# Kernel tuning notes

Measured on AMD Instinct MI355X. Metric: run time of the kernel, lower is better.

The kernel has to match this reference:

```python
import jax, jax.numpy as jnp
import numpy as np

N_NODES = 100000
N_EDGES = 2000000
FEAT = 4
H = 64
L = 3  # num_mp_layers
E = 2  # edge_types


def _p(key, shape, scale=0.05):
    return jax.random.normal(key, shape, dtype=jnp.float32) * scale


def setup_inputs() -> dict:
    key = jax.random.key(0)
    ks = jax.random.split(key, 24)
    inp = {
        "x": jax.random.normal(ks[0], (N_NODES, FEAT), dtype=jnp.float32),
        "node_type": jax.random.randint(ks[1], (N_NODES,), 0, 3),
        "edge_index": jax.random.randint(ks[2], (2, N_EDGES), 0, N_NODES),
        "edge_type": jax.random.randint(ks[3], (N_EDGES,), 0, E),
        # input_proj: Linear(4,64) + LayerNorm(64)
        "in_w": _p(ks[4], (FEAT, H)), "in_b": _p(ks[5], (H,)),
        "ln_g": jnp.ones((H,), jnp.float32), "ln_b": jnp.zeros((H,), jnp.float32),
        # per-layer, per-edge-type message MLPs: Linear(2H,H) -> ReLU -> Linear(H,H)
        "mlp_w1": _p(ks[6], (L, E, 2 * H, H)), "mlp_b1": _p(ks[7], (L, E, H)),
        "mlp_w2": _p(ks[8], (L, E, H, H)), "mlp_b2": _p(ks[9], (L, E, H)),
        # per-layer GRUCell(H,H): gates ordered [r, z, n] as in torch
        "gru_wi": _p(ks[10], (L, H, 3 * H)), "gru_wh": _p(ks[11], (L, H, 3 * H)),
        "gru_bi": _p(ks[12], (L, 3 * H)), "gru_bh": _p(ks[13], (L, 3 * H)),
        # readout: Linear(H,H) -> ReLU -> Linear(H,1)
        "ro_w1": _p(ks[14], (H, H)), "ro_b1": _p(ks[15], (H,)),
        "ro_w2": _p(ks[16], (H, 1)), "ro_b2": _p(ks[17], (1,)),
    }
    return inp


def _layernorm(h, g, b, eps=1e-5):
    mu = jnp.mean(h, axis=-1, keepdims=True)
    var = jnp.mean(jnp.square(h - mu), axis=-1, keepdims=True)
    return (h - mu) * jax.lax.rsqrt(var + eps) * g + b


def _forward(x, edge_index, edge_type, node_type,
             in_w, in_b, ln_g, ln_b,
             mlp_w1, mlp_b1, mlp_w2, mlp_b2,
             gru_wi, gru_wh, gru_bi, gru_bh,
             ro_w1, ro_b1, ro_w2, ro_b2):
    n = x.shape[0]
    # input projection (dropout is identity at inference)
    h = jax.nn.relu(_layernorm(x @ in_w + in_b, ln_g, ln_b))
    src, dst = edge_index[0], edge_index[1]
    for l in range(L):
        # gather -> concat: (M, 2H)
        mi = jnp.concatenate([h[src], h[dst]], axis=1)
        msg = jnp.zeros((mi.shape[0], H), dtype=h.dtype)
        for e in range(E):
            m = jax.nn.relu(mi @ mlp_w1[l, e] + mlp_b1[l, e]) @ mlp_w2[l, e] + mlp_b2[l, e]
            msg = msg + jnp.where((edge_type == e)[:, None], m, jnp.zeros((), h.dtype))
        # scatter_add over destination nodes
        agg = jax.ops.segment_sum(msg, dst, num_segments=n)
        # GRUCell(agg, h), torch gate order [r, z, n]
        gi = agg @ gru_wi[l] + gru_bi[l]
        gh = h @ gru_wh[l] + gru_bh[l]
        i_r, i_z, i_n = jnp.split(gi, 3, axis=-1)
        h_r, h_z, h_n = jnp.split(gh, 3, axis=-1)
        r = jax.nn.sigmoid(i_r + h_r)
        z = jax.nn.sigmoid(i_z + h_z)
        nn_ = jnp.tanh(i_n + r * h_n)
        h = (1.0 - z) * nn_ + z * h
    out = jax.nn.relu(h @ ro_w1 + ro_b1) @ ro_w2 + ro_b2  # (N, 1)
    # additive correction for data qubits (node_type==0); other nodes zeroed
    corr = jnp.where(node_type == 0, x[:, 0] + out[:, 0], jnp.zeros((), x.dtype))
    return corr


def reference(x, node_type, edge_index, edge_type,
              in_w, in_b, ln_g, ln_b,
              mlp_w1, mlp_b1, mlp_w2, mlp_b2,
              gru_wi, gru_wh, gru_bi, gru_bh,
              ro_w1, ro_b1, ro_w2, ro_b2):
    return _forward(x, edge_index, edge_type, node_type,
                    in_w, in_b, ln_g, ln_b,
                    mlp_w1, mlp_b1, mlp_w2, mlp_b2,
                    gru_wi, gru_wh, gru_bi, gru_bh,
                    ro_w1, ro_b1, ro_w2, ro_b2)
```

## Files before the change

### kernel.cpp

```cpp
#include <hip/hip_runtime.h>

typedef unsigned int u32;
typedef unsigned short u16;
typedef unsigned long long u64;

using short8 = __attribute__((ext_vector_type(8))) short;
using f32x4  = __attribute__((ext_vector_type(4))) float;

__device__ __forceinline__ u32 f2bf(float f) {
    u32 u = __float_as_uint(f);
    return (u + 0x7fffu + ((u >> 16) & 1u)) >> 16;
}
__device__ __forceinline__ u32 pk(float a, float b) {
    return f2bf(a) | (f2bf(b) << 16);
}
__device__ __forceinline__ u32 f2bf_fast(float f) {
    return (__float_as_uint(f) + 0x8000u) >> 16;
}
__device__ __forceinline__ u32 pk_fast(float a, float b) {
    return f2bf_fast(a) | (f2bf_fast(b) << 16);
}
__device__ __forceinline__ float bflo(u32 u) { return __uint_as_float(u << 16); }
__device__ __forceinline__ float bfhi(u32 u) { return __uint_as_float(u & 0xffff0000u); }
__device__ __forceinline__ float bfu(u16 u) { return __uint_as_float(((u32)u) << 16); }

union U8 { u32 u[4]; short8 v; };

__global__ void k_input_proj(const float* __restrict__ x, const float* __restrict__ in_w,
                             const float* __restrict__ in_b, const float* __restrict__ ln_g,
                             const float* __restrict__ ln_b, u16* __restrict__ hbf,
                             float* __restrict__ agg, int n_nodes, int nd8) {
    const int lane = threadIdx.x & 63;
    const int g = blockIdx.x & 7, ib = blockIdx.x >> 3;
    const int node = g * nd8 + ib * 4 + (threadIdx.x >> 6);
    if (node >= n_nodes || node >= (g + 1) * nd8) return;
    agg[(size_t)node * 64 + lane] = 0.f;
    float acc = in_b[lane];
#pragma unroll
    for (int k = 0; k < 4; ++k) acc = fmaf(x[node * 4 + k], in_w[k * 64 + lane], acc);
    float s = acc;
#pragma unroll
    for (int off = 32; off > 0; off >>= 1) s += __shfl_xor(s, off);
    float mu = s * (1.f / 64.f);
    float d = acc - mu;
    float vs = d * d;
#pragma unroll
    for (int off = 32; off > 0; off >>= 1) vs += __shfl_xor(vs, off);
    float inv = rsqrtf(vs * (1.f / 64.f) + 1e-5f);
    float hv = fmaxf(d * inv * ln_g[lane] + ln_b[lane], 0.f);
    hbf[(size_t)node * 64 + lane] = (u16)f2bf(hv);
}

__global__ void k_hist(const int* __restrict__ dst, const int* __restrict__ ety,
                       int* __restrict__ cnt, int* __restrict__ key, int M, int N) {
    int i = blockIdx.x * 256 + threadIdx.x;
    if (i < M) {
        int k = (ety[i] & 1) * N + dst[i];
        key[i] = k;
        atomicAdd(&cnt[k], 1);
    }
}

__global__ void k_scan1(int* __restrict__ data, int* __restrict__ part, int N) {
    __shared__ int s[1024];
    const int t = threadIdx.x;
    const int i = blockIdx.x * 1024 + t;
    int v = (i < N) ? data[i] : 0;
    s[t] = v;
    __syncthreads();
#pragma unroll
    for (int d = 1; d < 1024; d <<= 1) {
        int x = (t >= d) ? s[t - d] : 0;
        __syncthreads();
        s[t] += x;
        __syncthreads();
    }
    if (i < N) data[i] = s[t] - v;
    if (t == 1023) part[blockIdx.x] = s[1023];
}

__global__ void k_scan2(int* __restrict__ part, int nb) {
    const int l = threadIdx.x & 63;
    int base = 0;
    for (int s = 0; s < nb; s += 64) {
        int i = s + l;
        int orig = (i < nb) ? part[i] : 0;
        int x = orig;
#pragma unroll
        for (int off = 1; off < 64; off <<= 1) {
            int t = __shfl_up(x, off);
            if (l >= off) x += t;
        }
        if (i < nb) part[i] = base + x - orig;
        base += __shfl(x, 63);
    }
}

__global__ void k_scan3(int* __restrict__ data, const int* __restrict__ part, int N,
                        int saveIdx, int* __restrict__ slot) {
    int i = blockIdx.x * 1024 + threadIdx.x;
    if (i < N) {
        int v = data[i] + part[blockIdx.x];
        data[i] = v;
        if (i == saveIdx) slot[0] = v;
    }
}

__global__ void k_filldst(const int* __restrict__ off, int* __restrict__ dstP,
                          int NB, int N, int M) {
    int b = blockIdx.x * 256 + threadIdx.x;
    if (b >= NB) return;
    int s = off[b];
    int e = (b + 1 < NB) ? off[b + 1] : M;
    int d = (b >= N) ? b - N : b;
    for (int p = s; p < e; ++p) dstP[p] = d;
}

__global__ void k_scatter(const int* __restrict__ src, const int* __restrict__ key,
                          int* __restrict__ cursor, int* __restrict__ srcP,
                          int M, int N, int nd8) {
    const int g = blockIdx.x & 7;
    const int nb = gridDim.x >> 3;
    const int bi = blockIdx.x >> 3;
    for (int e = bi * 256 + threadIdx.x; e < M; e += nb * 256) {
        int k = key[e];
        int d = (k >= N) ? k - N : k;
        if (d / nd8 == g) {
            int pos = atomicAdd(&cursor[k], 1);
            srcP[pos] = src[e] & 0x3FFFFFFF;
        }
    }
}

__global__ __launch_bounds__(256, 2) void k_edge_mlp(
    const u16* __restrict__ hbf, const int* __restrict__ srcP, const int* __restrict__ dstP,
    const int* __restrict__ t0p, const float* __restrict__ w1, const float* __restrict__ b1,
    const float* __restrict__ w2, const float* __restrict__ b2,
    float* __restrict__ agg, int M, const int* __restrict__ offEnd, int N, int nd8) {
    __shared__ u16 sMsg[4][4864];

    const int tid = threadIdx.x;
    const int l = tid & 63, wv = tid >> 6;
    const int l15 = l & 15, quad = l >> 4;
    const f32x4 vz = {0.f, 0.f, 0.f, 0.f};

    const int T0 = *t0p;
    const int half = gridDim.x >> 1;
    const int ty = (blockIdx.x >= half) ? 1 : 0;
    const int sub = ty ? (int)blockIdx.x - half : (int)blockIdx.x;
    const int g = sub & 7;
    const int bi = sub >> 3;
    const int nbg = half >> 3;

    const int tyStart = ty ? T0 : 0;
    const int tyEnd = ty ? M : T0;
    const int k0 = g * nd8, k1 = (g + 1) * nd8;
    const int b0 = (k0 == 0) ? tyStart : ((k0 >= N) ? tyEnd : offEnd[ty * N + k0 - 1]);
    const int b1e = (k1 >= N) ? tyEnd : offEnd[ty * N + k1 - 1];

    const int n_tiles_ty = (tyEnd + 63) >> 6;
    const int tlo = b0 >> 6;
    const int thi = (k1 >= N) ? n_tiles_ty : (b1e >> 6);
    const int lo = tyStart;
    const int hi = tyEnd;
    const int range = thi - tlo;
    const int per = (range + nbg - 1) / nbg;
    const int c0 = tlo + bi * per;
    const int c1 = min(c0 + per, thi);

    short8 Bf1[4][4], Bf2[2][4];
    f32x4 b1i[4], b2i[4];
#pragma unroll
    for (int ni = 0; ni < 4; ++ni) {
        const int c = ni * 16 + l15;
        const float bb2 = b2[ty * 64 + c];
        b2i[ni] = f32x4{bb2, bb2, bb2, bb2};
#pragma unroll
        for (int r = 0; r < 4; ++r) b1i[ni][r] = b1[ty * 64 + ni * 16 + quad * 4 + r];
#pragma unroll
        for (int s = 0; s < 4; ++s) {
            U8 tmp;
            const float* wp = w1 + (size_t)ty * 8192 + (size_t)(s * 32 + quad * 8) * 64 + c;
#pragma unroll
            for (int jp = 0; jp < 4; ++jp) tmp.u[jp] = pk(wp[(2 * jp) * 64], wp[(2 * jp + 1) * 64]);
            Bf1[s][ni] = tmp.v;
        }
#pragma unroll
        for (int s = 0; s < 2; ++s) {
            U8 tmp;
#pragma unroll
            for (int w = 0; w < 4; ++w) {
                const int row = s * 32 + (w >> 1) * 16 + quad * 4 + (w & 1) * 2;
                const float* wp = w2 + (size_t)ty * 4096 + (size_t)row * 64 + c;
                tmp.u[w] = pk(wp[0], wp[64]);
            }
            Bf2[s][ni] = tmp.v;
        }
    }

    u16* msg = sMsg[wv];

    int t = c0 + wv;
    int mdc = -1;
    int msn = 0, mdn = -1;
    short8 a1[4][4];
    if (t < c1) {
        int ec = min((t << 6) + l, M - 1);
        int ms = srcP[ec];
        mdc = dstP[ec];
#pragma unroll
        for (int mi = 0; mi < 4; ++mi) {
            int rs = __shfl(ms, mi * 16 + l15);
            int rd = __shfl(mdc, mi * 16 + l15);
#pragma unroll
            for (int s = 0; s < 4; ++s) {
                const int row = (s < 2) ? rs : rd;
                a1[mi][s] = *(const short8*)(hbf + (size_t)row * 64 + (s & 1) * 32 + quad * 8);
            }
        }
        int ecn = min(((t + 4) << 6) + l, M - 1);
        msn = srcP[ecn];
        mdn = dstP[ecn];
    }

    for (; t < c1; t += 4) {
        const int base = t << 6;
        const int ecf = min(((t + 8) << 6) + l, M - 1);
        const int msf = srcP[ecf];
        const int mdf = dstP[ecf];

#pragma unroll
        for (int mi = 0; mi < 4; ++mi) {
            f32x4 acc[4] = {b1i[0], b1i[1], b1i[2], b1i[3]};
#pragma unroll
            for (int s = 0; s < 4; ++s)
#pragma unroll
                for (int ni = 0; ni < 4; ++ni)
                    acc[ni] = __builtin_amdgcn_mfma_f32_16x16x32_bf16(Bf1[s][ni], a1[mi][s], acc[ni], 0, 0, 0);
            {
                int rs = __shfl(msn, mi * 16 + l15);
                int rd = __shfl(mdn, mi * 16 + l15);
#pragma unroll
                for (int s = 0; s < 4; ++s) {
                    const int row = (s < 2) ? rs : rd;
                    a1[mi][s] = *(const short8*)(hbf + (size_t)row * 64 + (s & 1) * 32 + quad * 8);
                }
            }
            U8 pa, pb;
#pragma unroll
            for (int ni = 0; ni < 2; ++ni) {
                float h0 = fmaxf(acc[ni][0], 0.f);
                float h1 = fmaxf(acc[ni][1], 0.f);
                float h2 = fmaxf(acc[ni][2], 0.f);
                float h3 = fmaxf(acc[ni][3], 0.f);
                pa.u[ni * 2] = pk_fast(h0, h1);
                pa.u[ni * 2 + 1] = pk_fast(h2, h3);
            }
#pragma unroll
            for (int ni = 0; ni < 2; ++ni) {
                float h0 = fmaxf(acc[2 + ni][0], 0.f);
                float h1 = fmaxf(acc[2 + ni][1], 0.f);
                float h2 = fmaxf(acc[2 + ni][2], 0.f);
                float h3 = fmaxf(acc[2 + ni][3], 0.f);
                pb.u[ni * 2] = pk_fast(h0, h1);
                pb.u[ni * 2 + 1] = pk_fast(h2, h3);
            }
#pragma unroll
            for (int ni = 0; ni < 4; ++ni) {
                f32x4 tt = __builtin_amdgcn_mfma_f32_16x16x32_bf16(pa.v, Bf2[0][ni], b2i[ni], 0, 0, 0);
                f32x4 m2 = __builtin_amdgcn_mfma_f32_16x16x32_bf16(pb.v, Bf2[1][ni], tt, 0, 0, 0);
                const int c = ni * 16 + l15;
                const int e0 = mi * 16 + quad * 4;
                uint2 w;
                w.x = pk_fast(m2[0], m2[1]);
                w.y = pk_fast(m2[2], m2[3]);
                *(uint2*)(msg + c * 76 + e0) = w;
            }
        }

        {
            int eg = base + l;
            int dvz = (eg >= lo && eg < hi) ? mdc : -1;
            int dprev = __shfl_up(dvz, 1);
            u64 mask = __ballot((l == 0) || (dvz != dprev));
            mask |= (1ull << 16) | (1ull << 32) | (1ull << 48);
            float a = 0.f;
#pragma unroll
            for (int i = 0; i < 64; i += 4) {
                uint2 pr = *(const uint2*)(msg + l * 76 + i);
                float v0 = bflo(pr.x), v1 = bfhi(pr.x), v2 = bflo(pr.y), v3 = bfhi(pr.y);
#define RR_STEP(ii, vv)                                                         \
                a += (vv);                                                      \
                if ((ii) == 63 || ((mask >> ((ii) + 1)) & 1ull)) {              \
                    int dd = __builtin_amdgcn_readlane(dvz, (ii));              \
                    if (dd >= 0) unsafeAtomicAdd(agg + (size_t)dd * 64 + l, a); \
                    a = 0.f;                                                    \
                }
                RR_STEP(i, v0)
                RR_STEP(i + 1, v1)
                RR_STEP(i + 2, v2)
                RR_STEP(i + 3, v3)
#undef RR_STEP
            }
        }
        mdc = mdn;
        msn = msf;
        mdn = mdf;
    }
}

__global__ __launch_bounds__(256, 2) void k_gru_gemm(
    float* __restrict__ agg, u16* __restrict__ hbf,
    const float* __restrict__ wi, const float* __restrict__ wh,
    const float* __restrict__ bi, const float* __restrict__ bh, int n_nodes, int last,
    const float* __restrict__ ro_w1, const float* __restrict__ ro_b1,
    const float* __restrict__ ro_w2, const float* __restrict__ ro_b2,
    const float* __restrict__ x, const int* __restrict__ node_type, float* __restrict__ out) {
    extern __shared__ u16 smem[];
    u16* sRZ = smem;
    u16* sIN = smem + 128 * 136;
    u16* sHN = sIN + 64 * 72;
    u16* sTR = sHN + 64 * 72;
    u16* sRO = sTR + 4 * 16 * 72;

    const int tid = threadIdx.x;
    const int l = tid & 63, wv = tid >> 6;
    const int l15 = l & 15, quad = l >> 4;
    const f32x4 vz = {0.f, 0.f, 0.f, 0.f};

    for (int u = tid; u < 128 * 64; u += 256) {
        int c = u & 127, k0 = (u >> 7) * 2;
        float v0 = (k0 < 64) ? wi[k0 * 192 + c] : wh[(k0 - 64) * 192 + c];
        float v1 = (k0 < 64) ? wi[(k0 + 1) * 192 + c] : wh[(k0 + 1 - 64) * 192 + c];
        *(u32*)(sRZ + c * 136 + k0) = pk(v0, v1);
    }
    for (int u = tid; u < 64 * 32; u += 256) {
        int c = u & 63, k0 = (u >> 6) * 2;
        *(u32*)(sIN + c * 72 + k0) = pk(wi[k0 * 192 + 128 + c], wi[(k0 + 1) * 192 + 128 + c]);
        *(u32*)(sHN + c * 72 + k0) = pk(wh[k0 * 192 + 128 + c], wh[(k0 + 1) * 192 + 128 + c]);
        *(u32*)(sRO + c * 72 + k0) = pk(ro_w1[k0 * 64 + c], ro_w1[(k0 + 1) * 64 + c]);
    }
    float bR[4], bZ[4], bI[4], bH[4], b1v[4], w2v[4];
#pragma unroll
    for (int nt = 0; nt < 4; ++nt) {
        int j = nt * 16 + l15;
        bR[nt] = bi[j] + bh[j];
        bZ[nt] = bi[64 + j] + bh[64 + j];
        bI[nt] = bi[128 + j];
        bH[nt] = bh[128 + j];
        b1v[nt] = ro_b1[j];
        w2v[nt] = ro_w2[j];
    }
    const float b2s = ro_b2[0];
    __syncthreads();

    u16* tr = sTR + wv * (16 * 72);
    const f32x4 z4 = {0.f, 0.f, 0.f, 0.f};
    const int n_tiles = (n_nodes + 15) >> 4;
    const int g = blockIdx.x & 7, jb = blockIdx.x >> 3, nbg = gridDim.x >> 3;
    const int per8 = (n_tiles + 7) >> 3;
    const int glo = g * per8, ghi = min(glo + per8, n_tiles);
    for (int tile = glo + jb * 4 + wv; tile < ghi; tile += nbg * 4) {
        const int nb = tile << 4;
        const int arow = nb + l15;
        const int rowc = (arow < n_nodes) ? arow : (n_nodes - 1);
        short8 aA[2], aH[2];
#pragma unroll
        for (int s = 0; s < 2; ++s) {
            const float* ap = agg + (size_t)rowc * 64 + s * 32 + quad * 8;
            U8 tt;
#pragma unroll
            for (int jp = 0; jp < 4; ++jp) tt.u[jp] = pk(ap[2 * jp], ap[2 * jp + 1]);
            aA[s] = tt.v;
            aH[s] = *(const short8*)(hbf + (size_t)rowc * 64 + s * 32 + quad * 8);
        }
        if (!last && arow < n_nodes) {
#pragma unroll
            for (int s = 0; s < 2; ++s) {
                *(f32x4*)(agg + (size_t)rowc * 64 + s * 32 + quad * 8) = z4;
                *(f32x4*)(agg + (size_t)rowc * 64 + s * 32 + quad * 8 + 4) = z4;
            }
        }
        f32x4 D[16];
#pragma unroll
        for (int i = 0; i < 16; ++i) D[i] = vz;
#pragma unroll
        for (int nt = 0; nt < 8; ++nt) {
            const u16* bp = sRZ + (nt * 16 + l15) * 136 + quad * 8;
            D[nt] = __builtin_amdgcn_mfma_f32_16x16x32_bf16(aA[0], *(const short8*)bp, D[nt], 0, 0, 0);
            D[nt] = __builtin_amdgcn_mfma_f32_16x16x32_bf16(aA[1], *(const short8*)(bp + 32), D[nt], 0, 0, 0);
            D[nt] = __builtin_amdgcn_mfma_f32_16x16x32_bf16(aH[0], *(const short8*)(bp + 64), D[nt], 0, 0, 0);
            D[nt] = __builtin_amdgcn_mfma_f32_16x16x32_bf16(aH[1], *(const short8*)(bp + 96), D[nt], 0, 0, 0);
        }
#pragma unroll
        for (int nt = 0; nt < 4; ++nt) {
            const u16* ip = sIN + (nt * 16 + l15) * 72 + quad * 8;
            D[8 + nt] = __builtin_amdgcn_mfma_f32_16x16x32_bf16(aA[0], *(const short8*)ip, D[8 + nt], 0, 0, 0);
            D[8 + nt] = __builtin_amdgcn_mfma_f32_16x16x32_bf16(aA[1], *(const short8*)(ip + 32), D[8 + nt], 0, 0, 0);
            const u16* hp = sHN + (nt * 16 + l15) * 72 + quad * 8;
            D[12 + nt] = __builtin_amdgcn_mfma_f32_16x16x32_bf16(aH[0], *(const short8*)hp, D[12 + nt], 0, 0, 0);
            D[12 + nt] = __builtin_amdgcn_mfma_f32_16x16x32_bf16(aH[1], *(const short8*)(hp + 32), D[12 + nt], 0, 0, 0);
        }
#pragma unroll
        for (int nt = 0; nt < 4; ++nt) {
            const int j = nt * 16 + l15;
#pragma unroll
            for (int r = 0; r < 4; ++r) {
                const int nd = nb + quad * 4 + r;
                float rsv = D[nt][r] + bR[nt];
                float zsv = D[4 + nt][r] + bZ[nt];
                float inv = D[8 + nt][r] + bI[nt];
                float hnv = D[12 + nt][r] + bH[nt];
                float rr = 1.f / (1.f + __expf(-rsv));
                float zz = 1.f / (1.f + __expf(-zsv));
                float nn = tanhf(fmaf(rr, hnv, inv));
                float hv = (nd < n_nodes) ? bfu(hbf[(size_t)nd * 64 + j]) : 0.f;
                float nh = (1.f - zz) * nn + zz * hv;
                tr[(quad * 4 + r) * 72 + j] = (u16)f2bf(nh);
            }
        }
        {
            const int nd = nb + (l >> 2);
            if (nd < n_nodes) {
                const u16* sp = tr + (l >> 2) * 72 + (l & 3) * 16;
                uint4 va = *(const uint4*)sp;
                uint4 vb = *(const uint4*)(sp + 8);
                u16* dp = hbf + (size_t)nd * 64 + (l & 3) * 16;
                *(uint4*)dp = va;
                *(uint4*)(dp + 8) = vb;
            }
        }
        if (last) {
            short8 ar0 = *(const short8*)(tr + l15 * 72 + quad * 8);
            short8 ar1 = *(const short8*)(tr + l15 * 72 + 32 + quad * 8);
            float p[4] = {0.f, 0.f, 0.f, 0.f};
#pragma unroll
            for (int nt = 0; nt < 4; ++nt) {
                const u16* bp = sRO + (nt * 16 + l15) * 72 + quad * 8;
                f32x4 acc = __builtin_amdgcn_mfma_f32_16x16x32_bf16(ar0, *(const short8*)bp, vz, 0, 0, 0);
                acc = __builtin_amdgcn_mfma_f32_16x16x32_bf16(ar1, *(const short8*)(bp + 32), acc, 0, 0, 0);
#pragma unroll
                for (int r = 0; r < 4; ++r)
                    p[r] += fmaxf(acc[r] + b1v[nt], 0.f) * w2v[nt];
            }
#pragma unroll
            for (int off = 1; off < 16; off <<= 1)
#pragma unroll
                for (int r = 0; r < 4; ++r) p[r] += __shfl_xor(p[r], off);
            if (l15 == 0) {
#pragma unroll
                for (int r = 0; r < 4; ++r) {
                    const int nd = nb + quad * 4 + r;
                    if (nd < n_nodes) {
                        float o = p[r] + b2s;
                        out[nd] = (node_type[nd] == 0) ? (x[nd * 4] + o) : 0.f;
                    }
                }
            }
        }
    }
}

extern "C" void kernel_launch(void* const* d_in, const int* in_sizes, int n_in, void* d_out,
                              int out_size, void* d_ws, size_t ws_size, hipStream_t stream) {
    const float* x = (const float*)d_in[0];
    const int* node_type = (const int*)d_in[1];
    const int* edge_index = (const int*)d_in[2];
    const int* edge_type = (const int*)d_in[3];
    const float* in_w = (const float*)d_in[4];
    const float* in_b = (const float*)d_in[5];
    const float* ln_g = (const float*)d_in[6];
    const float* ln_b = (const float*)d_in[7];
    const float* mlp_w1 = (const float*)d_in[8];
    const float* mlp_b1 = (const float*)d_in[9];
    const float* mlp_w2 = (const float*)d_in[10];
    const float* mlp_b2 = (const float*)d_in[11];
    const float* gru_wi = (const float*)d_in[12];
    const float* gru_wh = (const float*)d_in[13];
    const float* gru_bi = (const float*)d_in[14];
    const float* gru_bh = (const float*)d_in[15];
    const float* ro_w1 = (const float*)d_in[16];
    const float* ro_b1 = (const float*)d_in[17];
    const float* ro_w2 = (const float*)d_in[18];
    const float* ro_b2 = (const float*)d_in[19];

    const int N = in_sizes[1];
    const int M = in_sizes[3];
    const int* src = edge_index;
    const int* dst = edge_index + M;

    char* wsb = (char*)d_ws;
    float* agg = (float*)wsb;
    u16* hbf = (u16*)(wsb + (size_t)N * 256);
    int* off = (int*)(wsb + (size_t)N * 384);
    int* part = (int*)(wsb + (size_t)N * 384 + (size_t)2 * N * 4);
    int* srcP = (int*)(wsb + (size_t)N * 384 + (size_t)2 * N * 4 + 4096);
    int* dstP = srcP + M;
    int* key = dstP + M;
    int* t0slot = part + 1000;

    const int NB = 2 * N;
    const int nb = (NB + 1023) / 1024;
    const int nd8 = (N + 7) / 8;

    hipMemsetAsync(off, 0, (size_t)NB * sizeof(int), stream);
    k_hist<<<(M + 255) / 256, 256, 0, stream>>>(dst, edge_type, off, key, M, N);
    k_scan1<<<nb, 1024, 0, stream>>>(off, part, NB);
    k_scan2<<<1, 64, 0, stream>>>(part, nb);
    k_scan3<<<nb, 1024, 0, stream>>>(off, part, NB, N, t0slot);
    k_filldst<<<(NB + 255) / 256, 256, 0, stream>>>(off, dstP, NB, N, M);
    k_scatter<<<2048, 256, 0, stream>>>(src, key, off, srcP, M, N, nd8);

    k_input_proj<<<8 * ((nd8 + 3) / 4), 256, 0, stream>>>(x, in_w, in_b, ln_g, ln_b, hbf, agg, N, nd8);
    const size_t gruLds =
        (size_t)(128 * 136 + 64 * 72 + 64 * 72 + 4 * 16 * 72 + 64 * 72) * sizeof(u16);
    for (int l = 0; l < 3; ++l) {
        k_edge_mlp<<<1024, 256, 0, stream>>>(hbf, srcP, dstP, t0slot,
                                             mlp_w1 + (size_t)l * 2 * 128 * 64,
                                             mlp_b1 + (size_t)l * 2 * 64,
                                             mlp_w2 + (size_t)l * 2 * 64 * 64,
                                             mlp_b2 + (size_t)l * 2 * 64, agg, M, off, N, nd8);
        k_gru_gemm<<<1024, 256, gruLds, stream>>>(agg, hbf, gru_wi + (size_t)l * 64 * 192,
                                                  gru_wh + (size_t)l * 64 * 192,
                                                  gru_bi + (size_t)l * 192, gru_bh + (size_t)l * 192,
                                                  N, (l == 2) ? 1 : 0,
                                                  ro_w1, ro_b1, ro_w2, ro_b2,
                                                  x, node_type, (float*)d_out);
    }
}
```

Before: 784.5 us.

## Replace atomic float aggregation with per-wave segment-aligned bf16 stores

Each wave now gets a contiguous edge range from a new binary-search split kernel, and the ranges are snapped to destination-segment boundaries. Each destination's sum can then be written once with a plain store instead of float atomics, and a carry register handles segments that span 64-edge tiles. Aggregates are kept in two bf16 buffers, one per edge type, and the GRU kernel sums them through extra MFMA passes. This drops atomic traffic and halves aggregate bandwidth, at the cost of a small extra launch, a second aggregate buffer to zero and read, and possible load imbalance for very large segments.

```diff
diff --git a/kernel.cpp b/kernel.cpp
--- a/kernel.cpp
+++ b/kernel.cpp
@@ -29,12 +29,16 @@
 __global__ void k_input_proj(const float* __restrict__ x, const float* __restrict__ in_w,
                              const float* __restrict__ in_b, const float* __restrict__ ln_g,
                              const float* __restrict__ ln_b, u16* __restrict__ hbf,
-                             float* __restrict__ agg, int n_nodes, int nd8) {
+                             u16* __restrict__ aggB, int n_nodes) {
     const int lane = threadIdx.x & 63;
-    const int g = blockIdx.x & 7, ib = blockIdx.x >> 3;
-    const int node = g * nd8 + ib * 4 + (threadIdx.x >> 6);
-    if (node >= n_nodes || node >= (g + 1) * nd8) return;
-    agg[(size_t)node * 64 + lane] = 0.f;
+    const int node = blockIdx.x * 4 + (threadIdx.x >> 6);
+    if (node >= n_nodes) return;
+    {
+        u32* r0 = (u32*)(aggB + (size_t)node * 64);
+        u32* r1 = (u32*)(aggB + ((size_t)n_nodes + node) * 64);
+        if (lane < 32) r0[lane] = 0u;
+        else r1[lane - 32] = 0u;
+    }
     float acc = in_b[lane];
 #pragma unroll
     for (int k = 0; k < 4; ++k) acc = fmaf(x[node * 4 + k], in_w[k * 64 + lane], acc);
@@ -114,6 +118,23 @@
     int e = (b + 1 < NB) ? off[b + 1] : M;
     int d = (b >= N) ? b - N : b;
     for (int p = s; p < e; ++p) dstP[p] = d;
+}
+
+__global__ void k_wsplit(const int* __restrict__ starts, int* __restrict__ wEdg,
+                         int N, int M) {
+    int i = blockIdx.x * 256 + threadIdx.x;
+    if (i >= 2 * 2049) return;
+    int t = i / 2049, w = i % 2049;
+    int lo = (t == 0) ? 0 : starts[N];
+    int hi = (t == 0) ? starts[N] : M;
+    if (w == 2048) { wEdg[i] = hi; return; }
+    long long target = lo + (long long)(hi - lo) * w / 2048;
+    int a = t * N, b = t * N + N;
+    while (b - a > 1) {
+        int m = (a + b) >> 1;
+        if ((long long)starts[m] <= target) a = m; else b = m;
+    }
+    wEdg[i] = starts[a];
 }
 
 __global__ void k_scatter(const int* __restrict__ src, const int* __restrict__ key,
@@ -134,39 +155,22 @@
 
 __global__ __launch_bounds__(256, 2) void k_edge_mlp(
     const u16* __restrict__ hbf, const int* __restrict__ srcP, const int* __restrict__ dstP,
-    const int* __restrict__ t0p, const float* __restrict__ w1, const float* __restrict__ b1,
+    const float* __restrict__ w1, const float* __restrict__ b1,
     const float* __restrict__ w2, const float* __restrict__ b2,
-    float* __restrict__ agg, int M, const int* __restrict__ offEnd, int N, int nd8) {
+    u16* __restrict__ aggB, int M, const int* __restrict__ wEdg, int N) {
     __shared__ u16 sMsg[4][4864];
 
     const int tid = threadIdx.x;
     const int l = tid & 63, wv = tid >> 6;
     const int l15 = l & 15, quad = l >> 4;
-    const f32x4 vz = {0.f, 0.f, 0.f, 0.f};
-
-    const int T0 = *t0p;
+
     const int half = gridDim.x >> 1;
     const int ty = (blockIdx.x >= half) ? 1 : 0;
     const int sub = ty ? (int)blockIdx.x - half : (int)blockIdx.x;
-    const int g = sub & 7;
-    const int bi = sub >> 3;
-    const int nbg = half >> 3;
-
-    const int tyStart = ty ? T0 : 0;
-    const int tyEnd = ty ? M : T0;
-    const int k0 = g * nd8, k1 = (g + 1) * nd8;
-    const int b0 = (k0 == 0) ? tyStart : ((k0 >= N) ? tyEnd : offEnd[ty * N + k0 - 1]);
-    const int b1e = (k1 >= N) ? tyEnd : offEnd[ty * N + k1 - 1];
-
-    const int n_tiles_ty = (tyEnd + 63) >> 6;
-    const int tlo = b0 >> 6;
-    const int thi = (k1 >= N) ? n_tiles_ty : (b1e >> 6);
-    const int lo = tyStart;
-    const int hi = tyEnd;
-    const int range = thi - tlo;
-    const int per = (range + nbg - 1) / nbg;
-    const int c0 = tlo + bi * per;
-    const int c1 = min(c0 + per, thi);
+    const int wl = sub * 4 + wv;
+    const int e0 = wEdg[ty * 2049 + wl];
+    const int e1 = wEdg[ty * 2049 + wl + 1];
+    u16* aggT = aggB + (size_t)ty * N * 64;
 
     short8 Bf1[4][4], Bf2[2][4];
     f32x4 b1i[4], b2i[4];
@@ -199,13 +203,13 @@
     }
 
     u16* msg = sMsg[wv];
-
-    int t = c0 + wv;
-    int mdc = -1;
-    int msn = 0, mdn = -1;
+    const int nT = (e1 - e0 + 63) >> 6;
+
+    int mdc = 0;
+    int msn = 0, mdn = 0;
     short8 a1[4][4];
-    if (t < c1) {
-        int ec = min((t << 6) + l, M - 1);
+    if (nT > 0) {
+        int ec = min(e0 + l, M - 1);
         int ms = srcP[ec];
         mdc = dstP[ec];
 #pragma unroll
@@ -218,14 +222,15 @@
                 a1[mi][s] = *(const short8*)(hbf + (size_t)row * 64 + (s & 1) * 32 + quad * 8);
             }
         }
-        int ecn = min(((t + 4) << 6) + l, M - 1);
+        int ecn = min(e0 + 64 + l, M - 1);
         msn = srcP[ecn];
         mdn = dstP[ecn];
     }
 
-    for (; t < c1; t += 4) {
-        const int base = t << 6;
-        const int ecf = min(((t + 8) << 6) + l, M - 1);
+    float carry = 0.f;
+    for (int j = 0; j < nT; ++j) {
+        const int base = e0 + (j << 6);
+        const int ecf = min(base + 128 + l, M - 1);
         const int msf = srcP[ecf];
         const int mdf = dstP[ecf];
 
@@ -270,30 +275,37 @@
                 f32x4 tt = __builtin_amdgcn_mfma_f32_16x16x32_bf16(pa.v, Bf2[0][ni], b2i[ni], 0, 0, 0);
                 f32x4 m2 = __builtin_amdgcn_mfma_f32_16x16x32_bf16(pb.v, Bf2[1][ni], tt, 0, 0, 0);
                 const int c = ni * 16 + l15;
-                const int e0 = mi * 16 + quad * 4;
+                const int e0v = mi * 16 + quad * 4;
                 uint2 w;
                 w.x = pk_fast(m2[0], m2[1]);
                 w.y = pk_fast(m2[2], m2[3]);
-                *(uint2*)(msg + c * 76 + e0) = w;
+                *(uint2*)(msg + c * 76 + e0v) = w;
             }
         }
 
         {
-            int eg = base + l;
-            int dvz = (eg >= lo && eg < hi) ? mdc : -1;
-            int dprev = __shfl_up(dvz, 1);
-            u64 mask = __ballot((l == 0) || (dvz != dprev));
-            mask |= (1ull << 16) | (1ull << 32) | (1ull << 48);
-            float a = 0.f;
+            const int eg = base + l;
+            const int dvz = (eg < e1) ? mdc : -1;
+            const int dprev = __shfl_up(dvz, 1);
+            const u64 mask = __ballot((l == 0) || (dvz != dprev));
+            const int dnext = (base + 64 < e1) ? __shfl(mdn, 0) : -1;
+            float a = carry;
+            carry = 0.f;
 #pragma unroll
             for (int i = 0; i < 64; i += 4) {
                 uint2 pr = *(const uint2*)(msg + l * 76 + i);
                 float v0 = bflo(pr.x), v1 = bfhi(pr.x), v2 = bflo(pr.y), v3 = bfhi(pr.y);
 #define RR_STEP(ii, vv)                                                         \
                 a += (vv);                                                      \
-                if ((ii) == 63 || ((mask >> ((ii) + 1)) & 1ull)) {              \
+                if ((ii) == 63) {                                               \
+                    int dd = __builtin_amdgcn_readlane(dvz, 63);                \
+                    if (dd >= 0) {                                              \
+                        if (dd == dnext) carry = a;                             \
+                        else aggT[(size_t)dd * 64 + l] = (u16)f2bf(a);          \
+                    }                                                           \
+                } else if ((mask >> ((ii) + 1)) & 1ull) {                       \
                     int dd = __builtin_amdgcn_readlane(dvz, (ii));              \
-                    if (dd >= 0) unsafeAtomicAdd(agg + (size_t)dd * 64 + l, a); \
+                    if (dd >= 0) aggT[(size_t)dd * 64 + l] = (u16)f2bf(a);      \
                     a = 0.f;                                                    \
                 }
                 RR_STEP(i, v0)
@@ -310,7 +322,7 @@
 }
 
 __global__ __launch_bounds__(256, 2) void k_gru_gemm(
-    float* __restrict__ agg, u16* __restrict__ hbf,
+    u16* __restrict__ aggB, u16* __restrict__ hbf,
     const float* __restrict__ wi, const float* __restrict__ wh,
     const float* __restrict__ bi, const float* __restrict__ bh, int n_nodes, int last,
     const float* __restrict__ ro_w1, const float* __restrict__ ro_b1,
@@ -355,7 +367,6 @@
     __syncthreads();
 
     u16* tr = sTR + wv * (16 * 72);
-    const f32x4 z4 = {0.f, 0.f, 0.f, 0.f};
     const int n_tiles = (n_nodes + 15) >> 4;
     const int g = blockIdx.x & 7, jb = blockIdx.x >> 3, nbg = gridDim.x >> 3;
     const int per8 = (n_tiles + 7) >> 3;
@@ -364,21 +375,19 @@
         const int nb = tile << 4;
         const int arow = nb + l15;
         const int rowc = (arow < n_nodes) ? arow : (n_nodes - 1);
-        short8 aA[2], aH[2];
+        short8 aA0[2], aA1[2], aH[2];
 #pragma unroll
         for (int s = 0; s < 2; ++s) {
-            const float* ap = agg + (size_t)rowc * 64 + s * 32 + quad * 8;
-            U8 tt;
-#pragma unroll
-            for (int jp = 0; jp < 4; ++jp) tt.u[jp] = pk(ap[2 * jp], ap[2 * jp + 1]);
-            aA[s] = tt.v;
-            aH[s] = *(const short8*)(hbf + (size_t)rowc * 64 + s * 32 + quad * 8);
+            aA0[s] = *(const short8*)(aggB + (size_t)rowc * 64 + s * 32 + quad * 8);
+            aA1[s] = *(const short8*)(aggB + ((size_t)n_nodes + rowc) * 64 + s * 32 + quad * 8);
+            aH[s]  = *(const short8*)(hbf + (size_t)rowc * 64 + s * 32 + quad * 8);
         }
         if (!last && arow < n_nodes) {
+            const uint4 z16 = {0u, 0u, 0u, 0u};
 #pragma unroll
             for (int s = 0; s < 2; ++s) {
-                *(f32x4*)(agg + (size_t)rowc * 64 + s * 32 + quad * 8) = z4;
-                *(f32x4*)(agg + (size_t)rowc * 64 + s * 32 + quad * 8 + 4) = z4;
+                *(uint4*)(aggB + (size_t)rowc * 64 + s * 32 + quad * 8) = z16;
+                *(uint4*)(aggB + ((size_t)n_nodes + rowc) * 64 + s * 32 + quad * 8) = z16;
             }
         }
         f32x4 D[16];
@@ -387,16 +396,20 @@
 #pragma unroll
         for (int nt = 0; nt < 8; ++nt) {
             const u16* bp = sRZ + (nt * 16 + l15) * 136 + quad * 8;
-            D[nt] = __builtin_amdgcn_mfma_f32_16x16x32_bf16(aA[0], *(const short8*)bp, D[nt], 0, 0, 0);
-            D[nt] = __builtin_amdgcn_mfma_f32_16x16x32_bf16(aA[1], *(const short8*)(bp + 32), D[nt], 0, 0, 0);
+            D[nt] = __builtin_amdgcn_mfma_f32_16x16x32_bf16(aA0[0], *(const short8*)bp, D[nt], 0, 0, 0);
+            D[nt] = __builtin_amdgcn_mfma_f32_16x16x32_bf16(aA0[1], *(const short8*)(bp + 32), D[nt], 0, 0, 0);
+            D[nt] = __builtin_amdgcn_mfma_f32_16x16x32_bf16(aA1[0], *(const short8*)bp, D[nt], 0, 0, 0);
+            D[nt] = __builtin_amdgcn_mfma_f32_16x16x32_bf16(aA1[1], *(const short8*)(bp + 32), D[nt], 0, 0, 0);
             D[nt] = __builtin_amdgcn_mfma_f32_16x16x32_bf16(aH[0], *(const short8*)(bp + 64), D[nt], 0, 0, 0);
             D[nt] = __builtin_amdgcn_mfma_f32_16x16x32_bf16(aH[1], *(const short8*)(bp + 96), D[nt], 0, 0, 0);
         }
 #pragma unroll
         for (int nt = 0; nt < 4; ++nt) {
             const u16* ip = sIN + (nt * 16 + l15) * 72 + quad * 8;
-            D[8 + nt] = __builtin_amdgcn_mfma_f32_16x16x32_bf16(aA[0], *(const short8*)ip, D[8 + nt], 0, 0, 0);
-            D[8 + nt] = __builtin_amdgcn_mfma_f32_16x16x32_bf16(aA[1], *(const short8*)(ip + 32), D[8 + nt], 0, 0, 0);
+            D[8 + nt] = __builtin_amdgcn_mfma_f32_16x16x32_bf16(aA0[0], *(const short8*)ip, D[8 + nt], 0, 0, 0);
+            D[8 + nt] = __builtin_amdgcn_mfma_f32_16x16x32_bf16(aA0[1], *(const short8*)(ip + 32), D[8 + nt], 0, 0, 0);
+            D[8 + nt] = __builtin_amdgcn_mfma_f32_16x16x32_bf16(aA1[0], *(const short8*)ip, D[8 + nt], 0, 0, 0);
+            D[8 + nt] = __builtin_amdgcn_mfma_f32_16x16x32_bf16(aA1[1], *(const short8*)(ip + 32), D[8 + nt], 0, 0, 0);
             const u16* hp = sHN + (nt * 16 + l15) * 72 + quad * 8;
             D[12 + nt] = __builtin_amdgcn_mfma_f32_16x16x32_bf16(aH[0], *(const short8*)hp, D[12 + nt], 0, 0, 0);
             D[12 + nt] = __builtin_amdgcn_mfma_f32_16x16x32_bf16(aH[1], *(const short8*)(hp + 32), D[12 + nt], 0, 0, 0);
@@ -490,13 +503,14 @@
     const int* dst = edge_index + M;
 
     char* wsb = (char*)d_ws;
-    float* agg = (float*)wsb;
+    u16* aggB = (u16*)wsb;
     u16* hbf = (u16*)(wsb + (size_t)N * 256);
     int* off = (int*)(wsb + (size_t)N * 384);
     int* part = (int*)(wsb + (size_t)N * 384 + (size_t)2 * N * 4);
     int* srcP = (int*)(wsb + (size_t)N * 384 + (size_t)2 * N * 4 + 4096);
     int* dstP = srcP + M;
     int* key = dstP + M;
+    int* wEdg = key + M;
     int* t0slot = part + 1000;
 
     const int NB = 2 * N;
@@ -509,18 +523,20 @@
     k_scan2<<<1, 64, 0, stream>>>(part, nb);
     k_scan3<<<nb, 1024, 0, stream>>>(off, part, NB, N, t0slot);
     k_filldst<<<(NB + 255) / 256, 256, 0, stream>>>(off, dstP, NB, N, M);
+    k_wsplit<<<(2 * 2049 + 255) / 256, 256, 0, stream>>>(off, wEdg, N, M);
     k_scatter<<<2048, 256, 0, stream>>>(src, key, off, srcP, M, N, nd8);
 
-    k_input_proj<<<8 * ((nd8 + 3) / 4), 256, 0, stream>>>(x, in_w, in_b, ln_g, ln_b, hbf, agg, N, nd8);
+    k_input_proj<<<(N + 3) / 4, 256, 0, stream>>>(x, in_w, in_b, ln_g, ln_b, hbf, aggB, N);
     const size_t gruLds =
         (size_t)(128 * 136 + 64 * 72 + 64 * 72 + 4 * 16 * 72 + 64 * 72) * sizeof(u16);
     for (int l = 0; l < 3; ++l) {
-        k_edge_mlp<<<1024, 256, 0, stream>>>(hbf, srcP, dstP, t0slot,
+        k_edge_mlp<<<1024, 256, 0, stream>>>(hbf, srcP, dstP,
                                              mlp_w1 + (size_t)l * 2 * 128 * 64,
                                              mlp_b1 + (size_t)l * 2 * 64,
                                              mlp_w2 + (size_t)l * 2 * 64 * 64,
-                                             mlp_b2 + (size_t)l * 2 * 64, agg, M, off, N, nd8);
-        k_gru_gemm<<<1024, 256, gruLds, stream>>>(agg, hbf, gru_wi + (size_t)l * 64 * 192,
+                                             mlp_b2 + (size_t)l * 2 * 64,
+                                             aggB, M, wEdg, N);
+        k_gru_gemm<<<1024, 256, gruLds, stream>>>(aggB, hbf, gru_wi + (size_t)l * 64 * 192,
                                                   gru_wh + (size_t)l * 64 * 192,
                                                   gru_bi + (size_t)l * 192, gru_bh + (size_t)l * 192,
                                                   N, (l == 2) ? 1 : 0,
```

New measurement: 781.3 us. No clear change (-0.4%).
